# Kernel optimization log

Hardware: AMD Instinct MI355X
Metric: run time of the kernel (lower is better)

## Reference

```python
import jax, jax.numpy as jnp
import numpy as np


def _lstm_cell(x, h, c, Wih, Whh, b):
    # PyTorch LSTMCell gate order: i, f, g, o; b = b_ih + b_hh
    z = x @ Wih.T + h @ Whh.T + b
    i, f, g, o = jnp.split(z, 4, axis=-1)
    c_new = jax.nn.sigmoid(f) * c + jax.nn.sigmoid(i) * jnp.tanh(g)
    h_new = jax.nn.sigmoid(o) * jnp.tanh(c_new)
    return h_new, c_new


B, T, F, H, HOR, OUT = 16384, 96, 16, 64, 24, 16


def setup_inputs() -> dict:
    key = jax.random.key(0)
    ks = jax.random.split(key, 20)
    s = 1.0 / np.sqrt(H)

    def u(k, shape):
        return jax.random.uniform(k, shape, jnp.float32, -s, s)

    return {
        "X": jax.random.normal(ks[0], (B, T, F), jnp.float32),
        "bias": jax.random.normal(ks[1], (B, 1, OUT), jnp.float32),
        "X_mask": jnp.ones((B, T), dtype=bool),
        # encoder layer 0 (in=F) and layer 1 (in=H)
        "enc_Wih0": u(ks[2], (4 * H, F)), "enc_Whh0": u(ks[3], (4 * H, H)), "enc_b0": u(ks[4], (4 * H,)),
        "enc_Wih1": u(ks[5], (4 * H, H)), "enc_Whh1": u(ks[6], (4 * H, H)), "enc_b1": u(ks[7], (4 * H,)),
        # decoder layers (in=H)
        "dec_Wih0": u(ks[8], (4 * H, H)), "dec_Whh0": u(ks[9], (4 * H, H)), "dec_b0": u(ks[10], (4 * H,)),
        "dec_Wih1": u(ks[11], (4 * H, H)), "dec_Whh1": u(ks[12], (4 * H, H)), "dec_b1": u(ks[13], (4 * H,)),
        "reg_W1": u(ks[14], (H, H)), "reg_b1": u(ks[15], (H,)),
        "reg_W2": u(ks[16], (OUT, H)), "reg_b2": u(ks[17], (OUT,)),
    }


def reference(X, bias, X_mask,
              enc_Wih0, enc_Whh0, enc_b0, enc_Wih1, enc_Whh1, enc_b1,
              dec_Wih0, dec_Whh0, dec_b0, dec_Wih1, dec_Whh1, dec_b1,
              reg_W1, reg_b1, reg_W2, reg_b2):
    b = X.shape[0]
    z = jnp.zeros((b, H), X.dtype)

    # ---- encoder: scan over time, 2 stacked LSTMCells ----
    def enc_step(carry, x_t):
        h0, c0, h1, c1 = carry
        h0, c0 = _lstm_cell(x_t, h0, c0, enc_Wih0, enc_Whh0, enc_b0)
        h1, c1 = _lstm_cell(h0, h1, c1, enc_Wih1, enc_Whh1, enc_b1)
        return (h0, c0, h1, c1), None

    (h0, _, h1, _), _ = jax.lax.scan(enc_step, (z, z, z, z),
                                     jnp.swapaxes(X, 0, 1))  # [T,B,F]

    # ---- decoder: fresh c (zeros), h from encoder, h_t starts at top-layer h ----
    last_bias = bias[:, -1]  # [B, OUT]

    def dec_step(carry, _):
        h_t, dh0, dc0, dh1, dc1 = carry
        h_t, dc0 = _lstm_cell(h_t, dh0, dc0, dec_Wih0, dec_Whh0, dec_b0)
        dh0 = h_t
        h_t, dc1 = _lstm_cell(h_t, dh1, dc1, dec_Wih1, dec_Whh1, dec_b1)
        dh1 = h_t
        y = jax.nn.relu(h_t @ reg_W1.T + reg_b1) @ reg_W2.T + reg_b2
        y = y + last_bias  # add_last_step_val=True
        return (h_t, dh0, dc0, dh1, dc1), y

    _, ys = jax.lax.scan(dec_step, (h1, h0, z, h1, z), None, length=HOR)
    return jnp.swapaxes(ys, 0, 1)  # [B, horizon, OUT]
```

## Files before the change

kernel.cpp:

```cpp
#include <hip/hip_runtime.h>

typedef short v8s __attribute__((ext_vector_type(8)));
typedef float v4f __attribute__((ext_vector_type(4)));

__device__ __forceinline__ unsigned cvtpk(float lo, float hi) {
    unsigned r;
    asm("v_cvt_pk_bf16_f32 %0, %1, %2" : "=v"(r) : "v"(lo), "v"(hi));
    return r;
}
__device__ __forceinline__ v8s pack8(float4 f0, float4 f1) {
    union { unsigned u[4]; v8s v; } r;
    r.u[0] = cvtpk(f0.x, f0.y); r.u[1] = cvtpk(f0.z, f0.w);
    r.u[2] = cvtpk(f1.x, f1.y); r.u[3] = cvtpk(f1.z, f1.w);
    return r.v;
}
__device__ __forceinline__ v4f mfma(v8s a, v8s b, v4f c) {
    return __builtin_amdgcn_mfma_f32_16x16x32_bf16(a, b, c, 0, 0, 0);
}
__device__ __forceinline__ v8s ldwf(const float* W, int rowElems, int n, int k0) {
    const float* p = W + (size_t)n * rowElems + k0;
    union { unsigned u[4]; v8s v; } r;
    #pragma unroll
    for (int j = 0; j < 4; ++j) r.u[j] = cvtpk(p[2 * j], p[2 * j + 1]);
    return r.v;
}

__device__ __forceinline__ float cell(float zi, float zf, float zg, float zo, float& c) {
    const float NL = -1.44269504f, PG = 2.88539008f;
    float ei = __builtin_amdgcn_exp2f(NL * zi);
    float ef = __builtin_amdgcn_exp2f(NL * zf);
    float eg = __builtin_amdgcn_exp2f(PG * zg);
    float Df = 1.f + ef;
    float Dig = (1.f + ei) * (1.f + eg);
    float cc = (c * Dig + Df * (eg - 1.f)) * __builtin_amdgcn_rcpf(Df * Dig);
    c = cc;
    float eo = __builtin_amdgcn_exp2f(NL * zo);
    float ec = __builtin_amdgcn_exp2f(fminf(PG * cc, 60.f));
    return (ec - 1.f) * __builtin_amdgcn_rcpf((1.f + eo) * (1.f + ec));
}

__global__ __launch_bounds__(256, 2) void seq2seq(
    const float* __restrict__ X,
    const float* __restrict__ bias,
    const float* __restrict__ eWih0, const float* __restrict__ eWhh0, const float* __restrict__ eb0,
    const float* __restrict__ eWih1, const float* __restrict__ eWhh1, const float* __restrict__ eb1,
    const float* __restrict__ dWih0, const float* __restrict__ dWhh0, const float* __restrict__ db0,
    const float* __restrict__ dWih1, const float* __restrict__ dWhh1, const float* __restrict__ db1,
    const float* __restrict__ rW1, const float* __restrict__ rb1,
    const float* __restrict__ rW2, const float* __restrict__ rb2,
    float* __restrict__ out)
{
    __shared__ __align__(16) short sh0[2][1024];
    __shared__ __align__(16) short sh1[2][1024];
    __shared__ __align__(16) short sy1[1024];

    const int tid  = threadIdx.x;
    const int lane = tid & 63;
    const int w    = tid >> 6;
    const int lo   = lane & 15, hi = lane >> 4;
    const int wg   = blockIdx.x;

    for (int i = tid; i < 512; i += 256) {
        ((int*)sh0)[512 + i] = 0;
        ((int*)sh1)[512 + i] = 0;
    }

    const int wsidx = (w >> 1) * 512 + (((2 * w) + (lo >> 3)) & 3) * 128 + hi * 32 + (lo & 7);

    v8s wf[4][4][2];
    float bz0[4], bz1[4];
    #pragma unroll
    for (int g = 0; g < 4; ++g) {
        const int n = (w + 4 * g) * 16 + lo;
        v8s z = {0, 0, 0, 0, 0, 0, 0, 0};
        wf[0][g][0] = (hi < 2) ? ldwf(eWih0, 16, n, (hi & 1) * 8) : z;
        wf[0][g][1] = z;
        #pragma unroll
        for (int kk = 0; kk < 2; ++kk) {
            wf[1][g][kk] = ldwf(eWhh0, 64, n, kk * 32 + hi * 8);
            wf[2][g][kk] = ldwf(eWih1, 64, n, kk * 32 + hi * 8);
            wf[3][g][kk] = ldwf(eWhh1, 64, n, kk * 32 + hi * 8);
        }
        bz0[g] = eb0[g * 64 + w * 16 + lo];
        bz1[g] = eb1[g * 64 + w * 16 + lo];
    }

    float c0[4] = {0.f, 0.f, 0.f, 0.f};
    float c1[4] = {0.f, 0.f, 0.f, 0.f};
    __syncthreads();

    const float* xb = X + (size_t)(wg * 16 + lo) * 1536 + (hi & 1) * 8;

    #pragma unroll 2
    for (int t = 0; t < 96; ++t) {
        const int pw = t & 1, pr = pw ^ 1;
        const float* p = xb + t * 16;
        const float4 xv0 = *(const float4*)p;
        const float4 xv1 = *(const float4*)(p + 4);
        v4f acc[4];
        #pragma unroll
        for (int g = 0; g < 4; ++g)
            acc[g] = (v4f){bz0[g], bz0[g], bz0[g], bz0[g]};
        #pragma unroll
        for (int kk = 0; kk < 2; ++kk) {
            const v8s ah = *(const v8s*)&sh0[pr][kk * 512 + lane * 8];
            #pragma unroll
            for (int g = 0; g < 4; ++g) acc[g] = mfma(ah, wf[1][g][kk], acc[g]);
        }
        {
            const v8s ax = pack8(xv0, xv1);
            #pragma unroll
            for (int g = 0; g < 4; ++g) acc[g] = mfma(ax, wf[0][g][0], acc[g]);
        }
        {
            float hh[4];
            #pragma unroll
            for (int q = 0; q < 4; ++q)
                hh[q] = cell(acc[0][q], acc[1][q], acc[2][q], acc[3][q], c0[q]);
            #pragma unroll
            for (int qp = 0; qp < 2; ++qp) {
                unsigned pk = cvtpk(hh[2 * qp], hh[2 * qp + 1]);
                short* b = &sh0[pw][wsidx + qp * 16];
                b[0] = (short)pk; b[8] = (short)(pk >> 16);
            }
        }
        __syncthreads();
        #pragma unroll
        for (int g = 0; g < 4; ++g)
            acc[g] = (v4f){bz1[g], bz1[g], bz1[g], bz1[g]};
        #pragma unroll
        for (int kk = 0; kk < 2; ++kk) {
            const v8s ah = *(const v8s*)&sh0[pw][kk * 512 + lane * 8];
            const v8s bh = *(const v8s*)&sh1[pr][kk * 512 + lane * 8];
            #pragma unroll
            for (int g = 0; g < 4; ++g) {
                acc[g] = mfma(ah, wf[2][g][kk], acc[g]);
                acc[g] = mfma(bh, wf[3][g][kk], acc[g]);
            }
        }
        {
            float hh[4];
            #pragma unroll
            for (int q = 0; q < 4; ++q)
                hh[q] = cell(acc[0][q], acc[1][q], acc[2][q], acc[3][q], c1[q]);
            #pragma unroll
            for (int qp = 0; qp < 2; ++qp) {
                unsigned pk = cvtpk(hh[2 * qp], hh[2 * qp + 1]);
                short* b = &sh1[pw][wsidx + qp * 16];
                b[0] = (short)pk; b[8] = (short)(pk >> 16);
            }
        }
    }
    __syncthreads();

    #pragma unroll
    for (int g = 0; g < 4; ++g) {
        const int n = (w + 4 * g) * 16 + lo;
        #pragma unroll
        for (int kk = 0; kk < 2; ++kk) {
            wf[0][g][kk] = ldwf(dWih0, 64, n, kk * 32 + hi * 8);
            wf[1][g][kk] = ldwf(dWhh0, 64, n, kk * 32 + hi * 8);
            wf[2][g][kk] = ldwf(dWih1, 64, n, kk * 32 + hi * 8);
            wf[3][g][kk] = ldwf(dWhh1, 64, n, kk * 32 + hi * 8);
        }
        bz0[g] = db0[g * 64 + w * 16 + lo];
        bz1[g] = db1[g * 64 + w * 16 + lo];
    }
    v8s w1f[2], w2f[2];
    #pragma unroll
    for (int kk = 0; kk < 2; ++kk) {
        w1f[kk] = ldwf(rW1, 64, w * 16 + lo, kk * 32 + hi * 8);
        w2f[kk] = ldwf(rW2, 64, lo, kk * 32 + hi * 8);
    }
    const float hb1 = rb1[w * 16 + lo];
    const float hb2 = rb2[lo];
    float lb[4];
    #pragma unroll
    for (int q = 0; q < 4; ++q) {
        lb[q] = bias[(size_t)(wg * 16 + hi * 4 + q) * 16 + lo];
        c0[q] = 0.f;
        c1[q] = 0.f;
    }

    #pragma unroll 2
    for (int s = 0; s < 24; ++s) {
        const int pw = s & 1, pr = pw ^ 1;
        v4f acc[4];
        #pragma unroll
        for (int g = 0; g < 4; ++g)
            acc[g] = (v4f){bz0[g], bz0[g], bz0[g], bz0[g]};
        #pragma unroll
        for (int kk = 0; kk < 2; ++kk) {
            const v8s ah = *(const v8s*)&sh1[pr][kk * 512 + lane * 8];
            const v8s bh = *(const v8s*)&sh0[pr][kk * 512 + lane * 8];
            #pragma unroll
            for (int g = 0; g < 4; ++g) {
                acc[g] = mfma(ah, wf[0][g][kk], acc[g]);
                acc[g] = mfma(bh, wf[1][g][kk], acc[g]);
            }
        }
        {
            float hh[4];
            #pragma unroll
            for (int q = 0; q < 4; ++q)
                hh[q] = cell(acc[0][q], acc[1][q], acc[2][q], acc[3][q], c0[q]);
            #pragma unroll
            for (int qp = 0; qp < 2; ++qp) {
                unsigned pk = cvtpk(hh[2 * qp], hh[2 * qp + 1]);
                short* b = &sh0[pw][wsidx + qp * 16];
                b[0] = (short)pk; b[8] = (short)(pk >> 16);
            }
        }
        __syncthreads();
        if (w == 0 && s > 0) {
            v4f a2 = (v4f){hb2, hb2, hb2, hb2};
            #pragma unroll
            for (int kk = 0; kk < 2; ++kk) {
                const v8s a = *(const v8s*)&sy1[kk * 512 + lane * 8];
                a2 = mfma(a, w2f[kk], a2);
            }
            #pragma unroll
            for (int q = 0; q < 4; ++q) {
                size_t row = (size_t)(wg * 16 + hi * 4 + q);
                out[row * 384 + (s - 1) * 16 + lo] = a2[q] + lb[q];
            }
        }
        #pragma unroll
        for (int g = 0; g < 4; ++g)
            acc[g] = (v4f){bz1[g], bz1[g], bz1[g], bz1[g]};
        #pragma unroll
        for (int kk = 0; kk < 2; ++kk) {
            const v8s ah = *(const v8s*)&sh0[pw][kk * 512 + lane * 8];
            const v8s bh = *(const v8s*)&sh1[pr][kk * 512 + lane * 8];
            #pragma unroll
            for (int g = 0; g < 4; ++g) {
                acc[g] = mfma(ah, wf[2][g][kk], acc[g]);
                acc[g] = mfma(bh, wf[3][g][kk], acc[g]);
            }
        }
        {
            float hh[4];
            #pragma unroll
            for (int q = 0; q < 4; ++q)
                hh[q] = cell(acc[0][q], acc[1][q], acc[2][q], acc[3][q], c1[q]);
            #pragma unroll
            for (int qp = 0; qp < 2; ++qp) {
                unsigned pk = cvtpk(hh[2 * qp], hh[2 * qp + 1]);
                short* b = &sh1[pw][wsidx + qp * 16];
                b[0] = (short)pk; b[8] = (short)(pk >> 16);
            }
        }
        __syncthreads();
        v4f ay = (v4f){hb1, hb1, hb1, hb1};
        #pragma unroll
        for (int kk = 0; kk < 2; ++kk) {
            const v8s ah = *(const v8s*)&sh1[pw][kk * 512 + lane * 8];
            ay = mfma(ah, w1f[kk], ay);
        }
        #pragma unroll
        for (int qp = 0; qp < 2; ++qp) {
            unsigned pk = cvtpk(fmaxf(ay[2 * qp], 0.f), fmaxf(ay[2 * qp + 1], 0.f));
            short* b = &sy1[wsidx + qp * 16];
            b[0] = (short)pk; b[8] = (short)(pk >> 16);
        }
    }
    __syncthreads();
    if (w == 0) {
        v4f a2 = (v4f){hb2, hb2, hb2, hb2};
        #pragma unroll
        for (int kk = 0; kk < 2; ++kk) {
            const v8s a = *(const v8s*)&sy1[kk * 512 + lane * 8];
            a2 = mfma(a, w2f[kk], a2);
        }
        #pragma unroll
        for (int q = 0; q < 4; ++q) {
            size_t row = (size_t)(wg * 16 + hi * 4 + q);
            out[row * 384 + 23 * 16 + lo] = a2[q] + lb[q];
        }
    }
}

extern "C" void kernel_launch(void* const* d_in, const int* in_sizes, int n_in,
                              void* d_out, int out_size, void* d_ws, size_t ws_size,
                              hipStream_t stream) {
    seq2seq<<<dim3(1024), dim3(256), 0, stream>>>(
        (const float*)d_in[0],
        (const float*)d_in[1],
        (const float*)d_in[3],  (const float*)d_in[4],  (const float*)d_in[5],
        (const float*)d_in[6],  (const float*)d_in[7],  (const float*)d_in[8],
        (const float*)d_in[9],  (const float*)d_in[10], (const float*)d_in[11],
        (const float*)d_in[12], (const float*)d_in[13], (const float*)d_in[14],
        (const float*)d_in[15], (const float*)d_in[16],
        (const float*)d_in[17], (const float*)d_in[18],
        (float*)d_out);
}
```

Measured before the change: 559.3 us.

## Split LSTM gate columns across two wave halves with LDS exchange

```diff
diff --git a/kernel.cpp b/kernel.cpp
--- a/kernel.cpp
+++ b/kernel.cpp
@@ -39,7 +39,7 @@
     return (ec - 1.f) * __builtin_amdgcn_rcpf((1.f + eo) * (1.f + ec));
 }
 
-__global__ __launch_bounds__(256, 2) void seq2seq(
+__global__ __launch_bounds__(512, 4) void seq2seq(
     const float* __restrict__ X,
     const float* __restrict__ bias,
     const float* __restrict__ eWih0, const float* __restrict__ eWhh0, const float* __restrict__ eb0,
@@ -52,41 +52,42 @@
 {
     __shared__ __align__(16) short sh0[2][1024];
     __shared__ __align__(16) short sh1[2][1024];
-    __shared__ __align__(16) short sy1[1024];
+    __shared__ __align__(16) short sy1[2][1024];
+    __shared__ __align__(16) v4f   zx[2][8][64];
 
     const int tid  = threadIdx.x;
     const int lane = tid & 63;
     const int w    = tid >> 6;
+    const int ug   = w & 3;
+    const int half = w >> 2;
     const int lo   = lane & 15, hi = lane >> 4;
     const int wg   = blockIdx.x;
 
-    for (int i = tid; i < 512; i += 256) {
-        ((int*)sh0)[512 + i] = 0;
-        ((int*)sh1)[512 + i] = 0;
-    }
-
-    const int wsidx = (w >> 1) * 512 + (((2 * w) + (lo >> 3)) & 3) * 128 + hi * 32 + (lo & 7);
-
-    v8s wf[4][4][2];
-    float bz0[4], bz1[4];
-    #pragma unroll
-    for (int g = 0; g < 4; ++g) {
-        const int n = (w + 4 * g) * 16 + lo;
+    ((int*)sh0)[512 + tid] = 0;
+    ((int*)sh1)[512 + tid] = 0;
+
+    const int wsidx = (ug >> 1) * 512 + (((2 * ug) + (lo >> 3)) & 3) * 128 + hi * 32 + (lo & 7);
+
+    v8s wX[2][2], wY[2][2], wZ[2][2], wW[2][2];
+    float bz0[2], bz1[2];
+    #pragma unroll
+    for (int a = 0; a < 2; ++a) {
+        const int n = (2 * half + a) * 64 + ug * 16 + lo;
         v8s z = {0, 0, 0, 0, 0, 0, 0, 0};
-        wf[0][g][0] = (hi < 2) ? ldwf(eWih0, 16, n, (hi & 1) * 8) : z;
-        wf[0][g][1] = z;
-        #pragma unroll
-        for (int kk = 0; kk < 2; ++kk) {
-            wf[1][g][kk] = ldwf(eWhh0, 64, n, kk * 32 + hi * 8);
-            wf[2][g][kk] = ldwf(eWih1, 64, n, kk * 32 + hi * 8);
-            wf[3][g][kk] = ldwf(eWhh1, 64, n, kk * 32 + hi * 8);
-        }
-        bz0[g] = eb0[g * 64 + w * 16 + lo];
-        bz1[g] = eb1[g * 64 + w * 16 + lo];
-    }
-
-    float c0[4] = {0.f, 0.f, 0.f, 0.f};
-    float c1[4] = {0.f, 0.f, 0.f, 0.f};
+        wX[a][0] = (hi < 2) ? ldwf(eWih0, 16, n, (hi & 1) * 8) : z;
+        wX[a][1] = z;
+        #pragma unroll
+        for (int kk = 0; kk < 2; ++kk) {
+            wY[a][kk] = ldwf(eWhh0, 64, n, kk * 32 + hi * 8);
+            wZ[a][kk] = ldwf(eWih1, 64, n, kk * 32 + hi * 8);
+            wW[a][kk] = ldwf(eWhh1, 64, n, kk * 32 + hi * 8);
+        }
+        bz0[a] = eb0[n];
+        bz1[a] = eb1[n];
+    }
+
+    float c0[2] = {0.f, 0.f};
+    float c1[2] = {0.f, 0.f};
     __syncthreads();
 
     const float* xb = X + (size_t)(wg * 16 + lo) * 1536 + (hi & 1) * 8;
@@ -97,126 +98,178 @@
         const float* p = xb + t * 16;
         const float4 xv0 = *(const float4*)p;
         const float4 xv1 = *(const float4*)(p + 4);
-        v4f acc[4];
-        #pragma unroll
-        for (int g = 0; g < 4; ++g)
-            acc[g] = (v4f){bz0[g], bz0[g], bz0[g], bz0[g]};
+        v4f acc[2];
+        #pragma unroll
+        for (int a = 0; a < 2; ++a) acc[a] = (v4f){bz0[a], bz0[a], bz0[a], bz0[a]};
         #pragma unroll
         for (int kk = 0; kk < 2; ++kk) {
             const v8s ah = *(const v8s*)&sh0[pr][kk * 512 + lane * 8];
             #pragma unroll
-            for (int g = 0; g < 4; ++g) acc[g] = mfma(ah, wf[1][g][kk], acc[g]);
+            for (int a = 0; a < 2; ++a) acc[a] = mfma(ah, wY[a][kk], acc[a]);
         }
         {
             const v8s ax = pack8(xv0, xv1);
             #pragma unroll
-            for (int g = 0; g < 4; ++g) acc[g] = mfma(ax, wf[0][g][0], acc[g]);
-        }
-        {
-            float hh[4];
-            #pragma unroll
-            for (int q = 0; q < 4; ++q)
-                hh[q] = cell(acc[0][q], acc[1][q], acc[2][q], acc[3][q], c0[q]);
-            #pragma unroll
-            for (int qp = 0; qp < 2; ++qp) {
-                unsigned pk = cvtpk(hh[2 * qp], hh[2 * qp + 1]);
-                short* b = &sh0[pw][wsidx + qp * 16];
-                b[0] = (short)pk; b[8] = (short)(pk >> 16);
-            }
-        }
-        __syncthreads();
-        #pragma unroll
-        for (int g = 0; g < 4; ++g)
-            acc[g] = (v4f){bz1[g], bz1[g], bz1[g], bz1[g]};
+            for (int a = 0; a < 2; ++a) acc[a] = mfma(ax, wX[a][0], acc[a]);
+        }
+        if (half) zx[0][w][lane] = (v4f){acc[0][0], acc[0][1], acc[1][0], acc[1][1]};
+        else      zx[0][w][lane] = (v4f){acc[0][2], acc[0][3], acc[1][2], acc[1][3]};
+        __syncthreads();
+        {
+            const v4f rx = zx[0][w ^ 4][lane];
+            float h0v, h1v;
+            if (half == 0) {
+                h0v = cell(acc[0][0], acc[1][0], rx[0], rx[2], c0[0]);
+                h1v = cell(acc[0][1], acc[1][1], rx[1], rx[3], c0[1]);
+            } else {
+                h0v = cell(rx[0], rx[2], acc[0][2], acc[1][2], c0[0]);
+                h1v = cell(rx[1], rx[3], acc[0][3], acc[1][3], c0[1]);
+            }
+            unsigned pk = cvtpk(h0v, h1v);
+            short* b = &sh0[pw][wsidx + half * 16];
+            b[0] = (short)pk; b[8] = (short)(pk >> 16);
+        }
+        __syncthreads();
+        #pragma unroll
+        for (int a = 0; a < 2; ++a) acc[a] = (v4f){bz1[a], bz1[a], bz1[a], bz1[a]};
         #pragma unroll
         for (int kk = 0; kk < 2; ++kk) {
             const v8s ah = *(const v8s*)&sh0[pw][kk * 512 + lane * 8];
             const v8s bh = *(const v8s*)&sh1[pr][kk * 512 + lane * 8];
             #pragma unroll
-            for (int g = 0; g < 4; ++g) {
-                acc[g] = mfma(ah, wf[2][g][kk], acc[g]);
-                acc[g] = mfma(bh, wf[3][g][kk], acc[g]);
-            }
-        }
-        {
-            float hh[4];
-            #pragma unroll
-            for (int q = 0; q < 4; ++q)
-                hh[q] = cell(acc[0][q], acc[1][q], acc[2][q], acc[3][q], c1[q]);
-            #pragma unroll
-            for (int qp = 0; qp < 2; ++qp) {
-                unsigned pk = cvtpk(hh[2 * qp], hh[2 * qp + 1]);
-                short* b = &sh1[pw][wsidx + qp * 16];
-                b[0] = (short)pk; b[8] = (short)(pk >> 16);
-            }
+            for (int a = 0; a < 2; ++a) {
+                acc[a] = mfma(ah, wZ[a][kk], acc[a]);
+                acc[a] = mfma(bh, wW[a][kk], acc[a]);
+            }
+        }
+        if (half) zx[1][w][lane] = (v4f){acc[0][0], acc[0][1], acc[1][0], acc[1][1]};
+        else      zx[1][w][lane] = (v4f){acc[0][2], acc[0][3], acc[1][2], acc[1][3]};
+        __syncthreads();
+        {
+            const v4f rx = zx[1][w ^ 4][lane];
+            float h0v, h1v;
+            if (half == 0) {
+                h0v = cell(acc[0][0], acc[1][0], rx[0], rx[2], c1[0]);
+                h1v = cell(acc[0][1], acc[1][1], rx[1], rx[3], c1[1]);
+            } else {
+                h0v = cell(rx[0], rx[2], acc[0][2], acc[1][2], c1[0]);
+                h1v = cell(rx[1], rx[3], acc[0][3], acc[1][3], c1[1]);
+            }
+            unsigned pk = cvtpk(h0v, h1v);
+            short* b = &sh1[pw][wsidx + half * 16];
+            b[0] = (short)pk; b[8] = (short)(pk >> 16);
         }
     }
     __syncthreads();
 
     #pragma unroll
-    for (int g = 0; g < 4; ++g) {
-        const int n = (w + 4 * g) * 16 + lo;
-        #pragma unroll
-        for (int kk = 0; kk < 2; ++kk) {
-            wf[0][g][kk] = ldwf(dWih0, 64, n, kk * 32 + hi * 8);
-            wf[1][g][kk] = ldwf(dWhh0, 64, n, kk * 32 + hi * 8);
-            wf[2][g][kk] = ldwf(dWih1, 64, n, kk * 32 + hi * 8);
-            wf[3][g][kk] = ldwf(dWhh1, 64, n, kk * 32 + hi * 8);
-        }
-        bz0[g] = db0[g * 64 + w * 16 + lo];
-        bz1[g] = db1[g * 64 + w * 16 + lo];
+    for (int a = 0; a < 2; ++a) {
+        const int n = (2 * half + a) * 64 + ug * 16 + lo;
+        #pragma unroll
+        for (int kk = 0; kk < 2; ++kk) {
+            wX[a][kk] = ldwf(dWih0, 64, n, kk * 32 + hi * 8);
+            wY[a][kk] = ldwf(dWhh0, 64, n, kk * 32 + hi * 8);
+            wZ[a][kk] = ldwf(dWih1, 64, n, kk * 32 + hi * 8);
+            wW[a][kk] = ldwf(dWhh1, 64, n, kk * 32 + hi * 8);
+        }
+        bz0[a] = db0[n];
+        bz1[a] = db1[n];
     }
     v8s w1f[2], w2f[2];
     #pragma unroll
     for (int kk = 0; kk < 2; ++kk) {
-        w1f[kk] = ldwf(rW1, 64, w * 16 + lo, kk * 32 + hi * 8);
+        w1f[kk] = ldwf(rW1, 64, ug * 16 + lo, kk * 32 + hi * 8);
         w2f[kk] = ldwf(rW2, 64, lo, kk * 32 + hi * 8);
     }
-    const float hb1 = rb1[w * 16 + lo];
+    const float hb1 = rb1[ug * 16 + lo];
     const float hb2 = rb2[lo];
     float lb[4];
     #pragma unroll
-    for (int q = 0; q < 4; ++q) {
-        lb[q] = bias[(size_t)(wg * 16 + hi * 4 + q) * 16 + lo];
-        c0[q] = 0.f;
-        c1[q] = 0.f;
-    }
+    for (int q = 0; q < 4; ++q) lb[q] = bias[(size_t)(wg * 16 + hi * 4 + q) * 16 + lo];
+    c0[0] = c0[1] = c1[0] = c1[1] = 0.f;
 
     #pragma unroll 2
     for (int s = 0; s < 24; ++s) {
         const int pw = s & 1, pr = pw ^ 1;
-        v4f acc[4];
-        #pragma unroll
-        for (int g = 0; g < 4; ++g)
-            acc[g] = (v4f){bz0[g], bz0[g], bz0[g], bz0[g]};
+        v4f acc[2];
+        #pragma unroll
+        for (int a = 0; a < 2; ++a) acc[a] = (v4f){bz0[a], bz0[a], bz0[a], bz0[a]};
         #pragma unroll
         for (int kk = 0; kk < 2; ++kk) {
             const v8s ah = *(const v8s*)&sh1[pr][kk * 512 + lane * 8];
             const v8s bh = *(const v8s*)&sh0[pr][kk * 512 + lane * 8];
             #pragma unroll
-            for (int g = 0; g < 4; ++g) {
-                acc[g] = mfma(ah, wf[0][g][kk], acc[g]);
-                acc[g] = mfma(bh, wf[1][g][kk], acc[g]);
-            }
-        }
-        {
-            float hh[4];
-            #pragma unroll
-            for (int q = 0; q < 4; ++q)
-                hh[q] = cell(acc[0][q], acc[1][q], acc[2][q], acc[3][q], c0[q]);
+            for (int a = 0; a < 2; ++a) {
+                acc[a] = mfma(ah, wX[a][kk], acc[a]);
+                acc[a] = mfma(bh, wY[a][kk], acc[a]);
+            }
+        }
+        if (half) zx[0][w][lane] = (v4f){acc[0][0], acc[0][1], acc[1][0], acc[1][1]};
+        else      zx[0][w][lane] = (v4f){acc[0][2], acc[0][3], acc[1][2], acc[1][3]};
+        __syncthreads();
+        {
+            const v4f rx = zx[0][w ^ 4][lane];
+            float h0v, h1v;
+            if (half == 0) {
+                h0v = cell(acc[0][0], acc[1][0], rx[0], rx[2], c0[0]);
+                h1v = cell(acc[0][1], acc[1][1], rx[1], rx[3], c0[1]);
+            } else {
+                h0v = cell(rx[0], rx[2], acc[0][2], acc[1][2], c0[0]);
+                h1v = cell(rx[1], rx[3], acc[0][3], acc[1][3], c0[1]);
+            }
+            unsigned pk = cvtpk(h0v, h1v);
+            short* b = &sh0[pw][wsidx + half * 16];
+            b[0] = (short)pk; b[8] = (short)(pk >> 16);
+        }
+        __syncthreads();
+        #pragma unroll
+        for (int a = 0; a < 2; ++a) acc[a] = (v4f){bz1[a], bz1[a], bz1[a], bz1[a]};
+        #pragma unroll
+        for (int kk = 0; kk < 2; ++kk) {
+            const v8s ah = *(const v8s*)&sh0[pw][kk * 512 + lane * 8];
+            const v8s bh = *(const v8s*)&sh1[pr][kk * 512 + lane * 8];
+            #pragma unroll
+            for (int a = 0; a < 2; ++a) {
+                acc[a] = mfma(ah, wZ[a][kk], acc[a]);
+                acc[a] = mfma(bh, wW[a][kk], acc[a]);
+            }
+        }
+        if (half) zx[1][w][lane] = (v4f){acc[0][0], acc[0][1], acc[1][0], acc[1][1]};
+        else      zx[1][w][lane] = (v4f){acc[0][2], acc[0][3], acc[1][2], acc[1][3]};
+        __syncthreads();
+        {
+            const v4f rx = zx[1][w ^ 4][lane];
+            float h0v, h1v;
+            if (half == 0) {
+                h0v = cell(acc[0][0], acc[1][0], rx[0], rx[2], c1[0]);
+                h1v = cell(acc[0][1], acc[1][1], rx[1], rx[3], c1[1]);
+            } else {
+                h0v = cell(rx[0], rx[2], acc[0][2], acc[1][2], c1[0]);
+                h1v = cell(rx[1], rx[3], acc[0][3], acc[1][3], c1[1]);
+            }
+            unsigned pk = cvtpk(h0v, h1v);
+            short* b = &sh1[pw][wsidx + half * 16];
+            b[0] = (short)pk; b[8] = (short)(pk >> 16);
+        }
+        __syncthreads();
+        if (w < 4) {
+            v4f ay = (v4f){hb1, hb1, hb1, hb1};
+            #pragma unroll
+            for (int kk = 0; kk < 2; ++kk) {
+                const v8s ah = *(const v8s*)&sh1[pw][kk * 512 + lane * 8];
+                ay = mfma(ah, w1f[kk], ay);
+            }
             #pragma unroll
             for (int qp = 0; qp < 2; ++qp) {
-                unsigned pk = cvtpk(hh[2 * qp], hh[2 * qp + 1]);
-                short* b = &sh0[pw][wsidx + qp * 16];
+                unsigned pk = cvtpk(fmaxf(ay[2 * qp], 0.f), fmaxf(ay[2 * qp + 1], 0.f));
+                short* b = &sy1[pw][wsidx + qp * 16];
                 b[0] = (short)pk; b[8] = (short)(pk >> 16);
             }
-        }
-        __syncthreads();
-        if (w == 0 && s > 0) {
+        } else if (w == 4 && s > 0) {
             v4f a2 = (v4f){hb2, hb2, hb2, hb2};
             #pragma unroll
             for (int kk = 0; kk < 2; ++kk) {
-                const v8s a = *(const v8s*)&sy1[kk * 512 + lane * 8];
+                const v8s a = *(const v8s*)&sy1[pr][kk * 512 + lane * 8];
                 a2 = mfma(a, w2f[kk], a2);
             }
             #pragma unroll
@@ -225,51 +278,13 @@
                 out[row * 384 + (s - 1) * 16 + lo] = a2[q] + lb[q];
             }
         }
-        #pragma unroll
-        for (int g = 0; g < 4; ++g)
-            acc[g] = (v4f){bz1[g], bz1[g], bz1[g], bz1[g]};
-        #pragma unroll
-        for (int kk = 0; kk < 2; ++kk) {
-            const v8s ah = *(const v8s*)&sh0[pw][kk * 512 + lane * 8];
-            const v8s bh = *(const v8s*)&sh1[pr][kk * 512 + lane * 8];
-            #pragma unroll
-            for (int g = 0; g < 4; ++g) {
-                acc[g] = mfma(ah, wf[2][g][kk], acc[g]);
-                acc[g] = mfma(bh, wf[3][g][kk], acc[g]);
-            }
-        }
-        {
-            float hh[4];
-            #pragma unroll
-            for (int q = 0; q < 4; ++q)
-                hh[q] = cell(acc[0][q], acc[1][q], acc[2][q], acc[3][q], c1[q]);
-            #pragma unroll
-            for (int qp = 0; qp < 2; ++qp) {
-                unsigned pk = cvtpk(hh[2 * qp], hh[2 * qp + 1]);
-                short* b = &sh1[pw][wsidx + qp * 16];
-                b[0] = (short)pk; b[8] = (short)(pk >> 16);
-            }
-        }
-        __syncthreads();
-        v4f ay = (v4f){hb1, hb1, hb1, hb1};
-        #pragma unroll
-        for (int kk = 0; kk < 2; ++kk) {
-            const v8s ah = *(const v8s*)&sh1[pw][kk * 512 + lane * 8];
-            ay = mfma(ah, w1f[kk], ay);
-        }
-        #pragma unroll
-        for (int qp = 0; qp < 2; ++qp) {
-            unsigned pk = cvtpk(fmaxf(ay[2 * qp], 0.f), fmaxf(ay[2 * qp + 1], 0.f));
-            short* b = &sy1[wsidx + qp * 16];
-            b[0] = (short)pk; b[8] = (short)(pk >> 16);
-        }
     }
     __syncthreads();
-    if (w == 0) {
+    if (w == 4) {
         v4f a2 = (v4f){hb2, hb2, hb2, hb2};
         #pragma unroll
         for (int kk = 0; kk < 2; ++kk) {
-            const v8s a = *(const v8s*)&sy1[kk * 512 + lane * 8];
+            const v8s a = *(const v8s*)&sy1[1][kk * 512 + lane * 8];
             a2 = mfma(a, w2f[kk], a2);
         }
         #pragma unroll
@@ -283,7 +298,7 @@
 extern "C" void kernel_launch(void* const* d_in, const int* in_sizes, int n_in,
                               void* d_out, int out_size, void* d_ws, size_t ws_size,
                               hipStream_t stream) {
-    seq2seq<<<dim3(1024), dim3(256), 0, stream>>>(
+    seq2seq<<<dim3(1024), dim3(512), 0, stream>>>(
         (const float*)d_in[0],
         (const float*)d_in[1],
         (const float*)d_in[3],  (const float*)d_in[4],  (const float*)d_in[5],
```

Result: slower. 674.9 us (+20.7%).

## Skew encoder layers across timesteps to halve barriers per step

Applied to the files above, without the earlier changes.

```diff
diff --git a/kernel.cpp b/kernel.cpp
--- a/kernel.cpp
+++ b/kernel.cpp
@@ -60,26 +60,22 @@
     const int lo   = lane & 15, hi = lane >> 4;
     const int wg   = blockIdx.x;
 
-    for (int i = tid; i < 512; i += 256) {
-        ((int*)sh0)[512 + i] = 0;
-        ((int*)sh1)[512 + i] = 0;
-    }
+    for (int i = tid; i < 512; i += 256) ((int*)sh1)[512 + i] = 0;
 
     const int wsidx = (w >> 1) * 512 + (((2 * w) + (lo >> 3)) & 3) * 128 + hi * 32 + (lo & 7);
 
-    v8s wf[4][4][2];
+    v8s wx[4], wh[4][2], wi1[4][2], wh1[4][2];
     float bz0[4], bz1[4];
     #pragma unroll
     for (int g = 0; g < 4; ++g) {
         const int n = (w + 4 * g) * 16 + lo;
         v8s z = {0, 0, 0, 0, 0, 0, 0, 0};
-        wf[0][g][0] = (hi < 2) ? ldwf(eWih0, 16, n, (hi & 1) * 8) : z;
-        wf[0][g][1] = z;
-        #pragma unroll
-        for (int kk = 0; kk < 2; ++kk) {
-            wf[1][g][kk] = ldwf(eWhh0, 64, n, kk * 32 + hi * 8);
-            wf[2][g][kk] = ldwf(eWih1, 64, n, kk * 32 + hi * 8);
-            wf[3][g][kk] = ldwf(eWhh1, 64, n, kk * 32 + hi * 8);
+        wx[g] = (hi < 2) ? ldwf(eWih0, 16, n, (hi & 1) * 8) : z;
+        #pragma unroll
+        for (int kk = 0; kk < 2; ++kk) {
+            wh[g][kk]  = ldwf(eWhh0, 64, n, kk * 32 + hi * 8);
+            wi1[g][kk] = ldwf(eWih1, 64, n, kk * 32 + hi * 8);
+            wh1[g][kk] = ldwf(eWhh1, 64, n, kk * 32 + hi * 8);
         }
         bz0[g] = eb0[g * 64 + w * 16 + lo];
         bz1[g] = eb1[g * 64 + w * 16 + lo];
@@ -87,81 +83,103 @@
 
     float c0[4] = {0.f, 0.f, 0.f, 0.f};
     float c1[4] = {0.f, 0.f, 0.f, 0.f};
+
+    const float* xb = X + (size_t)(wg * 16 + lo) * 1536 + (hi & 1) * 8;
+
+    v4f acc0[4];
+    {
+        const v8s ax = pack8(*(const float4*)xb, *(const float4*)(xb + 4));
+        #pragma unroll
+        for (int g = 0; g < 4; ++g) {
+            acc0[g] = (v4f){bz0[g], bz0[g], bz0[g], bz0[g]};
+            acc0[g] = mfma(ax, wx[g], acc0[g]);
+        }
+        float hh[4];
+        #pragma unroll
+        for (int q = 0; q < 4; ++q)
+            hh[q] = cell(acc0[0][q], acc0[1][q], acc0[2][q], acc0[3][q], c0[q]);
+        #pragma unroll
+        for (int qp = 0; qp < 2; ++qp) {
+            unsigned pk = cvtpk(hh[2 * qp], hh[2 * qp + 1]);
+            short* b = &sh0[0][wsidx + qp * 16];
+            b[0] = (short)pk; b[8] = (short)(pk >> 16);
+        }
+    }
     __syncthreads();
-
-    const float* xb = X + (size_t)(wg * 16 + lo) * 1536 + (hi & 1) * 8;
 
     #pragma unroll 2
     for (int t = 0; t < 96; ++t) {
-        const int pw = t & 1, pr = pw ^ 1;
-        const float* p = xb + t * 16;
+        const int sA = t & 1, sB = sA ^ 1;
+        const int tn = (t < 95) ? t + 1 : 95;
+        const float* p = xb + tn * 16;
         const float4 xv0 = *(const float4*)p;
         const float4 xv1 = *(const float4*)(p + 4);
-        v4f acc[4];
+        v8s ah[2], bh[2];
+        #pragma unroll
+        for (int kk = 0; kk < 2; ++kk) {
+            ah[kk] = *(const v8s*)&sh0[sA][kk * 512 + lane * 8];
+            bh[kk] = *(const v8s*)&sh1[sB][kk * 512 + lane * 8];
+        }
+        v4f acc1[4];
         #pragma unroll
         for (int g = 0; g < 4; ++g)
-            acc[g] = (v4f){bz0[g], bz0[g], bz0[g], bz0[g]};
-        #pragma unroll
-        for (int kk = 0; kk < 2; ++kk) {
-            const v8s ah = *(const v8s*)&sh0[pr][kk * 512 + lane * 8];
-            #pragma unroll
-            for (int g = 0; g < 4; ++g) acc[g] = mfma(ah, wf[1][g][kk], acc[g]);
-        }
+            acc1[g] = (v4f){bz1[g], bz1[g], bz1[g], bz1[g]};
+        #pragma unroll
+        for (int kk = 0; kk < 2; ++kk)
+            #pragma unroll
+            for (int g = 0; g < 4; ++g) {
+                acc1[g] = mfma(ah[kk], wi1[g][kk], acc1[g]);
+                acc1[g] = mfma(bh[kk], wh1[g][kk], acc1[g]);
+            }
+        #pragma unroll
+        for (int g = 0; g < 4; ++g)
+            acc0[g] = (v4f){bz0[g], bz0[g], bz0[g], bz0[g]};
+        #pragma unroll
+        for (int kk = 0; kk < 2; ++kk)
+            #pragma unroll
+            for (int g = 0; g < 4; ++g) acc0[g] = mfma(ah[kk], wh[g][kk], acc0[g]);
         {
             const v8s ax = pack8(xv0, xv1);
             #pragma unroll
-            for (int g = 0; g < 4; ++g) acc[g] = mfma(ax, wf[0][g][0], acc[g]);
+            for (int g = 0; g < 4; ++g) acc0[g] = mfma(ax, wx[g], acc0[g]);
         }
         {
             float hh[4];
             #pragma unroll
             for (int q = 0; q < 4; ++q)
-                hh[q] = cell(acc[0][q], acc[1][q], acc[2][q], acc[3][q], c0[q]);
+                hh[q] = cell(acc1[0][q], acc1[1][q], acc1[2][q], acc1[3][q], c1[q]);
             #pragma unroll
             for (int qp = 0; qp < 2; ++qp) {
                 unsigned pk = cvtpk(hh[2 * qp], hh[2 * qp + 1]);
-                short* b = &sh0[pw][wsidx + qp * 16];
+                short* b = &sh1[sA][wsidx + qp * 16];
+                b[0] = (short)pk; b[8] = (short)(pk >> 16);
+            }
+        }
+        {
+            float hh[4];
+            #pragma unroll
+            for (int q = 0; q < 4; ++q)
+                hh[q] = cell(acc0[0][q], acc0[1][q], acc0[2][q], acc0[3][q], c0[q]);
+            #pragma unroll
+            for (int qp = 0; qp < 2; ++qp) {
+                unsigned pk = cvtpk(hh[2 * qp], hh[2 * qp + 1]);
+                short* b = &sh0[sB][wsidx + qp * 16];
                 b[0] = (short)pk; b[8] = (short)(pk >> 16);
             }
         }
         __syncthreads();
-        #pragma unroll
-        for (int g = 0; g < 4; ++g)
-            acc[g] = (v4f){bz1[g], bz1[g], bz1[g], bz1[g]};
-        #pragma unroll
-        for (int kk = 0; kk < 2; ++kk) {
-            const v8s ah = *(const v8s*)&sh0[pw][kk * 512 + lane * 8];
-            const v8s bh = *(const v8s*)&sh1[pr][kk * 512 + lane * 8];
-            #pragma unroll
-            for (int g = 0; g < 4; ++g) {
-                acc[g] = mfma(ah, wf[2][g][kk], acc[g]);
-                acc[g] = mfma(bh, wf[3][g][kk], acc[g]);
-            }
-        }
-        {
-            float hh[4];
-            #pragma unroll
-            for (int q = 0; q < 4; ++q)
-                hh[q] = cell(acc[0][q], acc[1][q], acc[2][q], acc[3][q], c1[q]);
-            #pragma unroll
-            for (int qp = 0; qp < 2; ++qp) {
-                unsigned pk = cvtpk(hh[2 * qp], hh[2 * qp + 1]);
-                short* b = &sh1[pw][wsidx + qp * 16];
-                b[0] = (short)pk; b[8] = (short)(pk >> 16);
-            }
-        }
-    }
-    __syncthreads();
-
+    }
+
+    v8s dX0[4][2], dH0[4][2], dX1[4][2], dH1[4][2];
     #pragma unroll
     for (int g = 0; g < 4; ++g) {
         const int n = (w + 4 * g) * 16 + lo;
         #pragma unroll
         for (int kk = 0; kk < 2; ++kk) {
-            wf[0][g][kk] = ldwf(dWih0, 64, n, kk * 32 + hi * 8);
-            wf[1][g][kk] = ldwf(dWhh0, 64, n, kk * 32 + hi * 8);
-            wf[2][g][kk] = ldwf(dWih1, 64, n, kk * 32 + hi * 8);
-            wf[3][g][kk] = ldwf(dWhh1, 64, n, kk * 32 + hi * 8);
+            dX0[g][kk] = ldwf(dWih0, 64, n, kk * 32 + hi * 8);
+            dH0[g][kk] = ldwf(dWhh0, 64, n, kk * 32 + hi * 8);
+            dX1[g][kk] = ldwf(dWih1, 64, n, kk * 32 + hi * 8);
+            dH1[g][kk] = ldwf(dWhh1, 64, n, kk * 32 + hi * 8);
         }
         bz0[g] = db0[g * 64 + w * 16 + lo];
         bz1[g] = db1[g * 64 + w * 16 + lo];
@@ -182,28 +200,48 @@
         c1[q] = 0.f;
     }
 
+    {
+        v8s ah[2], bh[2];
+        #pragma unroll
+        for (int kk = 0; kk < 2; ++kk) {
+            ah[kk] = *(const v8s*)&sh1[1][kk * 512 + lane * 8];
+            bh[kk] = *(const v8s*)&sh0[1][kk * 512 + lane * 8];
+        }
+        #pragma unroll
+        for (int g = 0; g < 4; ++g)
+            acc0[g] = (v4f){bz0[g], bz0[g], bz0[g], bz0[g]};
+        #pragma unroll
+        for (int kk = 0; kk < 2; ++kk)
+            #pragma unroll
+            for (int g = 0; g < 4; ++g) {
+                acc0[g] = mfma(ah[kk], dX0[g][kk], acc0[g]);
+                acc0[g] = mfma(bh[kk], dH0[g][kk], acc0[g]);
+            }
+    }
+
     #pragma unroll 2
     for (int s = 0; s < 24; ++s) {
         const int pw = s & 1, pr = pw ^ 1;
-        v4f acc[4];
-        #pragma unroll
-        for (int g = 0; g < 4; ++g)
-            acc[g] = (v4f){bz0[g], bz0[g], bz0[g], bz0[g]};
-        #pragma unroll
-        for (int kk = 0; kk < 2; ++kk) {
-            const v8s ah = *(const v8s*)&sh1[pr][kk * 512 + lane * 8];
-            const v8s bh = *(const v8s*)&sh0[pr][kk * 512 + lane * 8];
-            #pragma unroll
-            for (int g = 0; g < 4; ++g) {
-                acc[g] = mfma(ah, wf[0][g][kk], acc[g]);
-                acc[g] = mfma(bh, wf[1][g][kk], acc[g]);
-            }
+        v4f acc1[4];
+        {
+            v8s bh[2];
+            #pragma unroll
+            for (int kk = 0; kk < 2; ++kk)
+                bh[kk] = *(const v8s*)&sh1[pr][kk * 512 + lane * 8];
+            #pragma unroll
+            for (int g = 0; g < 4; ++g)
+                acc1[g] = (v4f){bz1[g], bz1[g], bz1[g], bz1[g]};
+            #pragma unroll
+            for (int kk = 0; kk < 2; ++kk)
+                #pragma unroll
+                for (int g = 0; g < 4; ++g)
+                    acc1[g] = mfma(bh[kk], dH1[g][kk], acc1[g]);
         }
         {
             float hh[4];
             #pragma unroll
             for (int q = 0; q < 4; ++q)
-                hh[q] = cell(acc[0][q], acc[1][q], acc[2][q], acc[3][q], c0[q]);
+                hh[q] = cell(acc0[0][q], acc0[1][q], acc0[2][q], acc0[3][q], c0[q]);
             #pragma unroll
             for (int qp = 0; qp < 2; ++qp) {
                 unsigned pk = cvtpk(hh[2 * qp], hh[2 * qp + 1]);
@@ -225,24 +263,20 @@
                 out[row * 384 + (s - 1) * 16 + lo] = a2[q] + lb[q];
             }
         }
-        #pragma unroll
-        for (int g = 0; g < 4; ++g)
-            acc[g] = (v4f){bz1[g], bz1[g], bz1[g], bz1[g]};
-        #pragma unroll
-        for (int kk = 0; kk < 2; ++kk) {
-            const v8s ah = *(const v8s*)&sh0[pw][kk * 512 + lane * 8];
-            const v8s bh = *(const v8s*)&sh1[pr][kk * 512 + lane * 8];
-            #pragma unroll
-            for (int g = 0; g < 4; ++g) {
-                acc[g] = mfma(ah, wf[2][g][kk], acc[g]);
-                acc[g] = mfma(bh, wf[3][g][kk], acc[g]);
-            }
-        }
-        {
+        {
+            v8s ah[2];
+            #pragma unroll
+            for (int kk = 0; kk < 2; ++kk)
+                ah[kk] = *(const v8s*)&sh0[pw][kk * 512 + lane * 8];
+            #pragma unroll
+            for (int kk = 0; kk < 2; ++kk)
+                #pragma unroll
+                for (int g = 0; g < 4; ++g)
+                    acc1[g] = mfma(ah[kk], dX1[g][kk], acc1[g]);
             float hh[4];
             #pragma unroll
             for (int q = 0; q < 4; ++q)
-                hh[q] = cell(acc[0][q], acc[1][q], acc[2][q], acc[3][q], c1[q]);
+                hh[q] = cell(acc1[0][q], acc1[1][q], acc1[2][q], acc1[3][q], c1[q]);
             #pragma unroll
             for (int qp = 0; qp < 2; ++qp) {
                 unsigned pk = cvtpk(hh[2 * qp], hh[2 * qp + 1]);
@@ -251,17 +285,32 @@
             }
         }
         __syncthreads();
-        v4f ay = (v4f){hb1, hb1, hb1, hb1};
-        #pragma unroll
-        for (int kk = 0; kk < 2; ++kk) {
-            const v8s ah = *(const v8s*)&sh1[pw][kk * 512 + lane * 8];
-            ay = mfma(ah, w1f[kk], ay);
-        }
-        #pragma unroll
-        for (int qp = 0; qp < 2; ++qp) {
-            unsigned pk = cvtpk(fmaxf(ay[2 * qp], 0.f), fmaxf(ay[2 * qp + 1], 0.f));
-            short* b = &sy1[wsidx + qp * 16];
-            b[0] = (short)pk; b[8] = (short)(pk >> 16);
+        {
+            v8s h1f[2], h0f[2];
+            #pragma unroll
+            for (int kk = 0; kk < 2; ++kk) {
+                h1f[kk] = *(const v8s*)&sh1[pw][kk * 512 + lane * 8];
+                h0f[kk] = *(const v8s*)&sh0[pw][kk * 512 + lane * 8];
+            }
+            v4f ay = (v4f){hb1, hb1, hb1, hb1};
+            #pragma unroll
+            for (int kk = 0; kk < 2; ++kk) ay = mfma(h1f[kk], w1f[kk], ay);
+            #pragma unroll
+            for (int qp = 0; qp < 2; ++qp) {
+                unsigned pk = cvtpk(fmaxf(ay[2 * qp], 0.f), fmaxf(ay[2 * qp + 1], 0.f));
+                short* b = &sy1[wsidx + qp * 16];
+                b[0] = (short)pk; b[8] = (short)(pk >> 16);
+            }
+            #pragma unroll
+            for (int g = 0; g < 4; ++g)
+                acc0[g] = (v4f){bz0[g], bz0[g], bz0[g], bz0[g]};
+            #pragma unroll
+            for (int kk = 0; kk < 2; ++kk)
+                #pragma unroll
+                for (int g = 0; g < 4; ++g) {
+                    acc0[g] = mfma(h1f[kk], dX0[g][kk], acc0[g]);
+                    acc0[g] = mfma(h0f[kk], dH0[g][kk], acc0[g]);
+                }
         }
     }
     __syncthreads();
```

New measurement: 551.2 us. About the same (-1.4%).
